# Kernel tuning notes

Measured on AMD Instinct MI355X. Metric: run time of the kernel, lower is better.

## Reference

```python
import jax, jax.numpy as jnp
import numpy as np

B, C, L = 256, 256, 512
EPS = 1e-5

def setup_inputs() -> dict:
    key = jax.random.key(0)
    k1, k2, k3, k4 = jax.random.split(key, 4)
    x = jax.random.normal(k1, (B, C, L), dtype=jnp.float32)
    idx = jax.random.randint(k2, (B, L), 0, L + 1, dtype=jnp.int32)  # L == pad slot
    # Conv1d(2C, C, 1): weight [C, 2C], bias [C]
    W = jax.random.normal(k3, (C, 2 * C), dtype=jnp.float32) * (1.0 / np.sqrt(2 * C))
    b = jax.random.normal(k4, (C,), dtype=jnp.float32) * 0.01
    return {"x": x, "idx": idx, "W": W, "b": b}

def reference(x, idx, W, b):
    # collect_neighbours: pad length dim with one zero column, gather per (b, l)
    x_pad = jnp.pad(x, ((0, 0), (0, 0), (0, 1)))            # [B, C, L+1]
    nbr = jnp.take_along_axis(x_pad, idx[:, None, :].astype(jnp.int32), axis=2)  # [B, C, L]
    cat = jnp.concatenate([x, nbr], axis=1)                 # [B, 2C, L]
    # 1x1 Conv1d == channel matmul
    y = jnp.einsum('oc,bcl->bol', W, cat) + b[None, :, None]  # [B, C, L]
    # InstanceNorm1d (affine=False): normalize over L per (b, c), biased var
    mu = jnp.mean(y, axis=2, keepdims=True)
    var = jnp.mean(jnp.square(y - mu), axis=2, keepdims=True)
    y = (y - mu) * jax.lax.rsqrt(var + EPS)
    return jax.nn.relu(y)
```

## Files before the change

kernel.cpp:

```cpp
#include <hip/hip_runtime.h>
#include <hip/hip_bf16.h>
#include <stdint.h>

typedef __bf16 bf16x8 __attribute__((ext_vector_type(8)));
typedef float  f32x4  __attribute__((ext_vector_type(4)));

__device__ __forceinline__ uint32_t cvt2(float a, float b) {
    __hip_bfloat162 h = __float22bfloat162_rn(make_float2(a, b));
    uint32_t u; __builtin_memcpy(&u, &h, 4); return u;
}
__device__ __forceinline__ float bflo(uint32_t u) { uint32_t t = u << 16;         float f; __builtin_memcpy(&f, &t, 4); return f; }
__device__ __forceinline__ float bfhi(uint32_t u) { uint32_t t = u & 0xffff0000u; float f; __builtin_memcpy(&f, &t, 4); return f; }
__device__ __forceinline__ int swz(int u) { return u ^ ((u >> 3) & 7); }

__device__ __forceinline__ void gload_lds16(const void* g, void* l) {
    __builtin_amdgcn_global_load_lds(
        (const __attribute__((address_space(1))) uint32_t*)g,
        (__attribute__((address_space(3))) uint32_t*)l,
        16, 0, 0);
}

__global__ __launch_bounds__(256, 4)
void pack_transpose(const float* __restrict__ x, const float* __restrict__ W,
                    unsigned short* __restrict__ xT, unsigned short* __restrict__ wT)
{
    const int tid = threadIdx.x;
    const int id  = blockIdx.x;
    if (id < 2048) {
        const int b  = ((id >> 6) << 3) + (id & 7);
        const int kc = (id >> 3) & 7;
        const int s2 = tid >> 6, l4 = tid & 63;
        const float* src0 = x + ((size_t)b << 17) + ((size_t)((kc << 5) + (s2 << 3)) << 9);
        unsigned short* dst0 = xT + (((size_t)(b << 5) + (kc << 2) + s2) << 12);
        #pragma unroll
        for (int lh = 0; lh < 2; ++lh) {
            const int l0 = (lh << 8) + (l4 << 2);
            f32x4 xr[8];
            #pragma unroll
            for (int j = 0; j < 8; ++j)
                xr[j] = __builtin_nontemporal_load((const f32x4*)(src0 + (j << 9) + l0));
            #pragma unroll
            for (int lv = 0; lv < 4; ++lv) {
                uint4 p;
                p.x = cvt2(xr[0][lv], xr[1][lv]);
                p.y = cvt2(xr[2][lv], xr[3][lv]);
                p.z = cvt2(xr[4][lv], xr[5][lv]);
                p.w = cvt2(xr[6][lv], xr[7][lv]);
                *(uint4*)(dst0 + ((l0 + lv) << 3)) = p;
            }
        }
    } else {
        const int og = id - 2048;
        const int r = tid & 63, sg = tid >> 6;
        const float* wrow = W + ((size_t)((og << 5) + (r & 31)) << 9) + ((r >> 5) << 8);
        #pragma unroll
        for (int ss = 0; ss < 8; ++ss) {
            const int s = (sg << 3) + ss;
            float4 f0 = *(const float4*)(wrow + (s << 3));
            float4 f1 = *(const float4*)(wrow + (s << 3) + 4);
            uint4 p;
            p.x = cvt2(f0.x, f0.y); p.y = cvt2(f0.z, f0.w);
            p.z = cvt2(f1.x, f1.y); p.w = cvt2(f1.z, f1.w);
            *(uint4*)(wT + (((((og << 5) + s) << 6) + r) << 3)) = p;
        }
    }
}

__global__ __launch_bounds__(256, 2)
void edge_gemm(const unsigned short* __restrict__ xT,
               const unsigned short* __restrict__ wT,
               const int* __restrict__ idx,
               float* __restrict__ out)
{
    __shared__ __align__(16) unsigned char smem[73728];
    unsigned short* y2 = (unsigned short*)smem;
    float* red         = (float*)(smem + 36864);

    const int tid  = threadIdx.x;
    const int wv   = tid >> 6;
    const int lane = tid & 63;
    const int m    = lane & 15;
    const int q    = lane >> 4;

    const int id  = blockIdx.x;
    const int rem = id & 63;
    const int b   = ((id >> 6) << 3) + (rem & 7);
    const int og  = rem >> 3;
    const int o0  = og << 5;

    const char* xb = (const char*)xT + ((size_t)b << 18);
    const char* wb = (const char*)wT + (og << 15);

    const int offS = (wv << 10) + (lane << 4);

    int iv[8];
    #pragma unroll
    for (int nt = 0; nt < 8; ++nt)
        iv[nt] = idx[((size_t)b << 9) + (wv << 7) + (nt << 4) + m];

    f32x4 acc[4][8];
    #pragma unroll
    for (int mt = 0; mt < 4; ++mt)
        #pragma unroll
        for (int nt = 0; nt < 8; ++nt)
            acc[mt][nt] = (f32x4){0.f, 0.f, 0.f, 0.f};

    {
        char* Bl = (char*)smem;
        #pragma unroll
        for (int i = 0; i < 8; ++i)
            gload_lds16(xb + (i << 12) + offS, Bl + (i << 12) + offS);
        gload_lds16(wb + offS, Bl + 32768 + offS);
    }
    __syncthreads();

    #pragma unroll
    for (int kc = 0; kc < 8; ++kc) {
        const int cur = kc & 1;
        if (kc < 7) {
            char* Bl = (char*)smem + (cur ^ 1) * 36864;
            const char* Bg = xb + ((kc + 1) << 15);
            #pragma unroll
            for (int i = 0; i < 8; ++i)
                gload_lds16(Bg + (i << 12) + offS, Bl + (i << 12) + offS);
            gload_lds16(wb + ((kc + 1) << 12) + offS, Bl + 32768 + offS);
        }

        const unsigned short* B0 = (const unsigned short*)(smem + cur * 36864);
        const unsigned short* A0 = B0 + 16384;
        bf16x8 av[4], bv[8];
        #pragma unroll
        for (int mt = 0; mt < 4; ++mt)
            av[mt] = *(const bf16x8*)(A0 + (q << 9) + (((mt << 4) + m) << 3));
        #pragma unroll
        for (int nt = 0; nt < 8; ++nt)
            bv[nt] = *(const bf16x8*)(B0 + (q << 12) + (((wv << 7) + (nt << 4) + m) << 3));
        #pragma unroll
        for (int mt = 0; mt < 4; ++mt)
            #pragma unroll
            for (int nt = 0; nt < 8; ++nt)
                acc[mt][nt] = __builtin_amdgcn_mfma_f32_16x16x32_bf16(av[mt], bv[nt], acc[mt][nt], 0, 0, 0);

        if (kc < 7) __syncthreads();
    }

    #pragma unroll
    for (int mt = 2; mt < 4; ++mt)
        #pragma unroll
        for (int nt = 0; nt < 8; ++nt) {
            int col  = (wv << 7) + (nt << 4) + m;
            int row0 = ((mt - 2) << 4) + (q << 2);
            uint2 p;
            p.x = cvt2(acc[mt][nt][0], acc[mt][nt][1]);
            p.y = cvt2(acc[mt][nt][2], acc[mt][nt][3]);
            *(uint2*)(y2 + col * 36 + row0) = p;
        }
    __syncthreads();

    float vvl[2][8][4];
    float s_[2][4], q_[2][4];
    #pragma unroll
    for (int mt = 0; mt < 2; ++mt)
        #pragma unroll
        for (int r4 = 0; r4 < 4; ++r4) { s_[mt][r4] = 0.f; q_[mt][r4] = 0.f; }

    #pragma unroll
    for (int nt = 0; nt < 8; ++nt) {
        int  c   = iv[nt];
        bool inb = (c < 512);
        int  cc  = inb ? c : 0;
        #pragma unroll
        for (int mt = 0; mt < 2; ++mt) {
            uint2 g = *(const uint2*)(y2 + cc * 36 + (mt << 4) + (q << 2));
            float gv[4];
            gv[0] = inb ? bflo(g.x) : 0.f;
            gv[1] = inb ? bfhi(g.x) : 0.f;
            gv[2] = inb ? bflo(g.y) : 0.f;
            gv[3] = inb ? bfhi(g.y) : 0.f;
            #pragma unroll
            for (int r4 = 0; r4 < 4; ++r4) {
                float val = acc[mt][nt][r4] + gv[r4];
                vvl[mt][nt][r4] = val;
                s_[mt][r4] += val;
                q_[mt][r4] += val * val;
            }
        }
    }

    #pragma unroll
    for (int mt = 0; mt < 2; ++mt)
        #pragma unroll
        for (int r4 = 0; r4 < 4; ++r4) {
            float s = s_[mt][r4], ss = q_[mt][r4];
            #pragma unroll
            for (int off = 1; off < 16; off <<= 1) {
                s  += __shfl_xor(s,  off, 64);
                ss += __shfl_xor(ss, off, 64);
            }
            if (m == 0) {
                int r = (mt << 4) + (q << 2) + r4;
                red[(r << 3) + (wv << 1)]     = s;
                red[(r << 3) + (wv << 1) + 1] = ss;
            }
        }
    __syncthreads();

    #pragma unroll
    for (int mt = 0; mt < 2; ++mt)
        #pragma unroll
        for (int r4 = 0; r4 < 4; ++r4) {
            int r = (mt << 4) + (q << 2) + r4;
            float S = red[(r << 3)]     + red[(r << 3) + 2] + red[(r << 3) + 4] + red[(r << 3) + 6];
            float Q = red[(r << 3) + 1] + red[(r << 3) + 3] + red[(r << 3) + 5] + red[(r << 3) + 7];
            float mu  = S * (1.0f / 512.0f);
            float var = Q * (1.0f / 512.0f) - mu * mu;
            float rs  = rsqrtf(var + 1e-5f);
            float* op = out + (((size_t)(b << 8) + o0 + r) << 9) + (wv << 7) + m;
            #pragma unroll
            for (int nt = 0; nt < 8; ++nt) {
                float t = (vvl[mt][nt][r4] - mu) * rs;
                __builtin_nontemporal_store(fmaxf(t, 0.0f), op + (nt << 4));
            }
        }
}

__global__ __launch_bounds__(256, 2)
void edgeconv_fused(const float* __restrict__ x,
                    const int*   __restrict__ idx,
                    const float* __restrict__ W,
                    float*       __restrict__ out)
{
    __shared__ __align__(16) unsigned char smem[65536];
    unsigned short* wlds = (unsigned short*)smem;
    unsigned short* xTl  = (unsigned short*)(smem + 32768);
    unsigned short* y2   = (unsigned short*)smem;
    float*          red  = (float*)(smem + 38912);

    const int tid  = threadIdx.x;
    const int wv   = tid >> 6;
    const int lane = tid & 63;
    const int m    = lane & 15;
    const int q    = lane >> 4;

    const int id  = blockIdx.x;
    const int rem = id & 63;
    const int b   = ((id >> 6) << 3) + (rem & 7);
    const int o0  = (rem >> 3) << 5;

    const float* xb = x + ((size_t)b << 17);

    #pragma unroll
    for (int i = 0; i < 16; ++i) {
        int r = (i << 2) + wv;
        const float4 f = *(const float4*)(W + ((size_t)(o0 + (r & 31)) << 9)
                                            + ((r >> 5) << 8) + (lane << 2));
        uint2 p; p.x = cvt2(f.x, f.y); p.y = cvt2(f.z, f.w);
        int sl = lane >> 1;
        *(uint2*)(wlds + (sl << 9) + ((swz(r) ^ (sl & 7)) << 3) + ((lane & 1) << 2)) = p;
    }

    f32x4 acc[4][8];
    #pragma unroll
    for (int mt = 0; mt < 4; ++mt)
        #pragma unroll
        for (int nt = 0; nt < 8; ++nt)
            acc[mt][nt] = (f32x4){0.f, 0.f, 0.f, 0.f};

    float4 xr0[8], xr1[8];
    auto loadg = [&](int kc, int g, float4* xr) {
        int gid = (g << 8) + tid;
        int s2  = gid >> 7;
        int l4  = gid & 127;
        const float* base = xb + ((size_t)((kc << 5) + (s2 << 3)) << 9) + (l4 << 2);
        #pragma unroll
        for (int j = 0; j < 8; ++j) xr[j] = *(const float4*)(base + (j << 9));
    };
    auto storeg = [&](int g, const float4* xr) {
        int gid = (g << 8) + tid;
        int s2  = gid >> 7;
        int l4  = gid & 127;
        #pragma unroll
        for (int lv = 0; lv < 4; ++lv) {
            int l = (l4 << 2) + lv;
            uint4 p;
            p.x = cvt2((&xr[0].x)[lv], (&xr[1].x)[lv]);
            p.y = cvt2((&xr[2].x)[lv], (&xr[3].x)[lv]);
            p.z = cvt2((&xr[4].x)[lv], (&xr[5].x)[lv]);
            p.w = cvt2((&xr[6].x)[lv], (&xr[7].x)[lv]);
            *(uint4*)(xTl + (s2 << 12) + (swz(l) << 3)) = p;
        }
    };

    loadg(0, 0, xr0);
    loadg(0, 1, xr1);
    storeg(0, xr0);
    storeg(1, xr1);
    __syncthreads();

    for (int kc = 0; kc < 8; ++kc) {
        if (kc < 7) loadg(kc + 1, 0, xr0);

        bf16x8 av[4], bv[8];
        #pragma unroll
        for (int mt = 0; mt < 4; ++mt) {
            int sl = (kc << 2) + q;
            av[mt] = *(const bf16x8*)(wlds + (sl << 9) + ((swz((mt << 4) + m) ^ (sl & 7)) << 3));
        }
        #pragma unroll
        for (int nt = 0; nt < 8; ++nt)
            bv[nt] = *(const bf16x8*)(xTl + (q << 12) + (swz((wv << 7) + (nt << 4) + m) << 3));

        #pragma unroll
        for (int mt = 0; mt < 4; ++mt)
            #pragma unroll
            for (int nt = 0; nt < 8; ++nt)
                acc[mt][nt] = __builtin_amdgcn_mfma_f32_16x16x32_bf16(av[mt], bv[nt], acc[mt][nt], 0, 0, 0);

        if (kc < 7) loadg(kc + 1, 1, xr1);
        __syncthreads();
        if (kc < 7) {
            storeg(0, xr0);
            storeg(1, xr1);
            __syncthreads();
        }
    }

    int iv[8];
    #pragma unroll
    for (int nt = 0; nt < 8; ++nt)
        iv[nt] = idx[((size_t)b << 9) + (wv << 7) + (nt << 4) + m];

    #pragma unroll
    for (int mt = 2; mt < 4; ++mt)
        #pragma unroll
        for (int nt = 0; nt < 8; ++nt) {
            int col  = (wv << 7) + (nt << 4) + m;
            int row0 = ((mt - 2) << 4) + (q << 2);
            uint2 p;
            p.x = cvt2(acc[mt][nt][0], acc[mt][nt][1]);
            p.y = cvt2(acc[mt][nt][2], acc[mt][nt][3]);
            *(uint2*)(y2 + col * 36 + row0) = p;
        }
    __syncthreads();

    float vvl[2][8][4];
    float s_[2][4], q_[2][4];
    #pragma unroll
    for (int mt = 0; mt < 2; ++mt)
        #pragma unroll
        for (int r4 = 0; r4 < 4; ++r4) { s_[mt][r4] = 0.f; q_[mt][r4] = 0.f; }

    #pragma unroll
    for (int nt = 0; nt < 8; ++nt) {
        int  c   = iv[nt];
        bool inb = (c < 512);
        int  cc  = inb ? c : 0;
        #pragma unroll
        for (int mt = 0; mt < 2; ++mt) {
            uint2 g = *(const uint2*)(y2 + cc * 36 + (mt << 4) + (q << 2));
            float gv[4];
            gv[0] = inb ? bflo(g.x) : 0.f;
            gv[1] = inb ? bfhi(g.x) : 0.f;
            gv[2] = inb ? bflo(g.y) : 0.f;
            gv[3] = inb ? bfhi(g.y) : 0.f;
            #pragma unroll
            for (int r4 = 0; r4 < 4; ++r4) {
                float val = acc[mt][nt][r4] + gv[r4];
                vvl[mt][nt][r4] = val;
                s_[mt][r4] += val;
                q_[mt][r4] += val * val;
            }
        }
    }

    #pragma unroll
    for (int mt = 0; mt < 2; ++mt)
        #pragma unroll
        for (int r4 = 0; r4 < 4; ++r4) {
            float s = s_[mt][r4], ss = q_[mt][r4];
            #pragma unroll
            for (int off = 1; off < 16; off <<= 1) {
                s  += __shfl_xor(s,  off, 64);
                ss += __shfl_xor(ss, off, 64);
            }
            if (m == 0) {
                int r = (mt << 4) + (q << 2) + r4;
                red[(r << 3) + (wv << 1)]     = s;
                red[(r << 3) + (wv << 1) + 1] = ss;
            }
        }
    __syncthreads();

    #pragma unroll
    for (int mt = 0; mt < 2; ++mt)
        #pragma unroll
        for (int r4 = 0; r4 < 4; ++r4) {
            int r = (mt << 4) + (q << 2) + r4;
            float S = red[(r << 3)]     + red[(r << 3) + 2] + red[(r << 3) + 4] + red[(r << 3) + 6];
            float Q = red[(r << 3) + 1] + red[(r << 3) + 3] + red[(r << 3) + 5] + red[(r << 3) + 7];
            float mu  = S * (1.0f / 512.0f);
            float var = Q * (1.0f / 512.0f) - mu * mu;
            float rs  = rsqrtf(var + 1e-5f);
            float* op = out + (((size_t)(b << 8) + o0 + r) << 9) + (wv << 7) + m;
            #pragma unroll
            for (int nt = 0; nt < 8; ++nt) {
                float t = (vvl[mt][nt][r4] - mu) * rs;
                op[nt << 4] = fmaxf(t, 0.0f);
            }
        }
}

extern "C" void kernel_launch(void* const* d_in, const int* in_sizes, int n_in,
                              void* d_out, int out_size, void* d_ws, size_t ws_size,
                              hipStream_t stream) {
    const float* x   = (const float*)d_in[0];
    const int*   idx = (const int*)  d_in[1];
    const float* W   = (const float*)d_in[2];
    float* out = (float*)d_out;

    const size_t xT_bytes = (size_t)256 * 32 * 512 * 8 * 2;
    const size_t wT_bytes = (size_t)8 * 32 * 64 * 8 * 2;

    if (ws_size >= xT_bytes + wT_bytes) {
        unsigned short* xT = (unsigned short*)d_ws;
        unsigned short* wT = (unsigned short*)((char*)d_ws + xT_bytes);
        pack_transpose<<<dim3(2056), dim3(256), 0, stream>>>(x, W, xT, wT);
        edge_gemm<<<dim3(2048), dim3(256), 0, stream>>>(xT, wT, idx, out);
    } else {
        edgeconv_fused<<<dim3(2048), dim3(256), 0, stream>>>(x, idx, W, out);
    }
}
```

Measured before the change: 287.8 us.

## Stage transpose writes through LDS, retune row stride, and use plain output stores

The pack kernel now writes converted bf16 tuples into a swizzled shared buffer, then writes them out as contiguous 16-byte rows per thread, so global stores become fully coalesced. The GEMM kernel's stage loads are refactored into a lambda with a simplified offset, the neighbour-gather scratch stride drops from 36 to 34 halves (the reduction buffer moves to match), and the final output stores switch from nontemporal to regular stores. These changes target store coalescing and LDS bank conflicts. In exchange the pack kernel gains extra barriers and shared-memory traffic, and the odd stride may misalign the 8-byte uint2 accesses.

```diff
diff --git a/kernel.cpp b/kernel.cpp
--- a/kernel.cpp
+++ b/kernel.cpp
@@ -27,11 +27,12 @@
     const int tid = threadIdx.x;
     const int id  = blockIdx.x;
     if (id < 2048) {
+        __shared__ __align__(16) uint4 lbuf[1024];
         const int b  = ((id >> 6) << 3) + (id & 7);
         const int kc = (id >> 3) & 7;
         const int s2 = tid >> 6, l4 = tid & 63;
         const float* src0 = x + ((size_t)b << 17) + ((size_t)((kc << 5) + (s2 << 3)) << 9);
-        unsigned short* dst0 = xT + (((size_t)(b << 5) + (kc << 2) + s2) << 12);
+        unsigned short* dstb = xT + (((size_t)(b << 5) + (kc << 2)) << 12);
         #pragma unroll
         for (int lh = 0; lh < 2; ++lh) {
             const int l0 = (lh << 8) + (l4 << 2);
@@ -39,6 +40,7 @@
             #pragma unroll
             for (int j = 0; j < 8; ++j)
                 xr[j] = __builtin_nontemporal_load((const f32x4*)(src0 + (j << 9) + l0));
+            if (lh) __syncthreads();
             #pragma unroll
             for (int lv = 0; lv < 4; ++lv) {
                 uint4 p;
@@ -46,7 +48,15 @@
                 p.y = cvt2(xr[2][lv], xr[3][lv]);
                 p.z = cvt2(xr[4][lv], xr[5][lv]);
                 p.w = cvt2(xr[6][lv], xr[7][lv]);
-                *(uint4*)(dst0 + ((l0 + lv) << 3)) = p;
+                int a = (s2 << 8) + (l4 << 2) + lv;
+                lbuf[a ^ ((a >> 3) & 7)] = p;
+            }
+            __syncthreads();
+            #pragma unroll
+            for (int i = 0; i < 4; ++i) {
+                int a = (i << 8) + tid;
+                uint4 v = lbuf[a ^ ((a >> 3) & 7)];
+                *(uint4*)(dstb + ((size_t)i << 12) + (((lh << 8) + tid) << 3)) = v;
             }
         }
     } else {
@@ -74,7 +84,7 @@
 {
     __shared__ __align__(16) unsigned char smem[73728];
     unsigned short* y2 = (unsigned short*)smem;
-    float* red         = (float*)(smem + 36864);
+    float* red         = (float*)(smem + 34816);
 
     const int tid  = threadIdx.x;
     const int wv   = tid >> 6;
@@ -91,7 +101,7 @@
     const char* xb = (const char*)xT + ((size_t)b << 18);
     const char* wb = (const char*)wT + (og << 15);
 
-    const int offS = (wv << 10) + (lane << 4);
+    const int offS = tid << 4;
 
     int iv[8];
     #pragma unroll
@@ -105,26 +115,22 @@
         for (int nt = 0; nt < 8; ++nt)
             acc[mt][nt] = (f32x4){0.f, 0.f, 0.f, 0.f};
 
-    {
-        char* Bl = (char*)smem;
+    auto stage = [&](int c, int bsel) {
+        char* Bl = (char*)smem + bsel * 36864;
+        const char* Bg = xb + ((size_t)c << 15);
         #pragma unroll
         for (int i = 0; i < 8; ++i)
-            gload_lds16(xb + (i << 12) + offS, Bl + (i << 12) + offS);
-        gload_lds16(wb + offS, Bl + 32768 + offS);
-    }
+            gload_lds16(Bg + (i << 12) + offS, Bl + (i << 12) + offS);
+        gload_lds16(wb + (c << 12) + offS, Bl + 32768 + offS);
+    };
+
+    stage(0, 0);
     __syncthreads();
 
     #pragma unroll
     for (int kc = 0; kc < 8; ++kc) {
         const int cur = kc & 1;
-        if (kc < 7) {
-            char* Bl = (char*)smem + (cur ^ 1) * 36864;
-            const char* Bg = xb + ((kc + 1) << 15);
-            #pragma unroll
-            for (int i = 0; i < 8; ++i)
-                gload_lds16(Bg + (i << 12) + offS, Bl + (i << 12) + offS);
-            gload_lds16(wb + ((kc + 1) << 12) + offS, Bl + 32768 + offS);
-        }
+        if (kc < 7) stage(kc + 1, cur ^ 1);
 
         const unsigned short* B0 = (const unsigned short*)(smem + cur * 36864);
         const unsigned short* A0 = B0 + 16384;
@@ -153,7 +159,7 @@
             uint2 p;
             p.x = cvt2(acc[mt][nt][0], acc[mt][nt][1]);
             p.y = cvt2(acc[mt][nt][2], acc[mt][nt][3]);
-            *(uint2*)(y2 + col * 36 + row0) = p;
+            *(uint2*)(y2 + col * 34 + row0) = p;
         }
     __syncthreads();
 
@@ -171,7 +177,7 @@
         int  cc  = inb ? c : 0;
         #pragma unroll
         for (int mt = 0; mt < 2; ++mt) {
-            uint2 g = *(const uint2*)(y2 + cc * 36 + (mt << 4) + (q << 2));
+            uint2 g = *(const uint2*)(y2 + cc * 34 + (mt << 4) + (q << 2));
             float gv[4];
             gv[0] = inb ? bflo(g.x) : 0.f;
             gv[1] = inb ? bfhi(g.x) : 0.f;
@@ -219,7 +225,7 @@
             #pragma unroll
             for (int nt = 0; nt < 8; ++nt) {
                 float t = (vvl[mt][nt][r4] - mu) * rs;
-                __builtin_nontemporal_store(fmaxf(t, 0.0f), op + (nt << 4));
+                op[nt << 4] = fmaxf(t, 0.0f);
             }
         }
 }
```

Result: slower. 296.1 us (+2.9%).
